# Optimization experiments

Hardware: AMD Instinct MI355X
Metric: run time of the kernel (lower is better)

The kernel has to match this reference:

```python
import jax, jax.numpy as jnp
import numpy as np

NEG = -1e9

def symmetric_quantize(x, bits=8):
    qmax = 2 ** (bits - 1) - 1
    scale = jnp.max(jnp.abs(x)) / qmax
    xq = jnp.clip(jnp.round(x / scale), -(qmax + 1), qmax)
    return xq * scale

def setup_inputs() -> dict:
    key = jax.random.key(0)
    k1, k2, k3, k4, k5 = jax.random.split(key, 5)
    B, S, D = 2, 2048, 1024
    hidden_states = jax.random.normal(k1, (B, S, D), dtype=jnp.float32)
    # additive causal mask [1,1,S,S]
    causal = jnp.tril(jnp.ones((S, S), dtype=bool))
    attention_mask = jnp.where(causal, 0.0, NEG).astype(jnp.float32)[None, None]
    # weights stored (out,in) as used by F.linear; pre-quantized at init (weight_bits=8)
    W_attn = symmetric_quantize(jax.random.normal(k2, (3 * D, D), dtype=jnp.float32) * 0.02)
    b_attn = jax.random.normal(k3, (3 * D,), dtype=jnp.float32) * 0.02
    W_proj = symmetric_quantize(jax.random.normal(k4, (D, D), dtype=jnp.float32) * 0.02)
    b_proj = jax.random.normal(k5, (D,), dtype=jnp.float32) * 0.02
    return {"hidden_states": hidden_states, "attention_mask": attention_mask,
            "W_attn": W_attn, "b_attn": b_attn, "W_proj": W_proj, "b_proj": b_proj}

def reference(hidden_states, attention_mask, W_attn, b_attn, W_proj, b_proj):
    B, S, D = hidden_states.shape
    H = 16
    hd = D // H
    scale = 1.0 / jnp.sqrt(jnp.float32(hd))
    qkv = jnp.einsum('bsd,ed->bse', hidden_states, W_attn) + b_attn  # [B,S,3D]
    q, k, v = jnp.split(qkv, 3, axis=-1)
    def split_heads(x):
        return x.reshape(B, S, H, hd).transpose(0, 2, 1, 3)  # [B,H,S,hd]
    q, k, v = split_heads(q), split_heads(k), split_heads(v)
    # KV-cache fake quant (kv_bits=8)
    k = symmetric_quantize(k)
    v = symmetric_quantize(v)
    present = (k, v)
    scores = jnp.einsum('bhqd,bhkd->bhqk', q, k) * scale + attention_mask
    probs = jax.nn.softmax(scores, axis=-1)  # dropout is identity in eval
    out = jnp.einsum('bhqk,bhkd->bhqd', probs, v)
    out = out.transpose(0, 2, 1, 3).reshape(B, S, D)
    out = symmetric_quantize(out)  # activation fake quant (act_bits=8)
    out = jnp.einsum('bsd,ed->bse', out, W_proj) + b_proj
    return (out, present)
```

## Files before the change

kernel.cpp:

```cpp
#include <hip/hip_runtime.h>
#include <stdint.h>


typedef __attribute__((ext_vector_type(8))) short short8;
typedef __attribute__((ext_vector_type(4))) float floatx4;

#define SSCALE 0.18033688011112042f
#define MASKVAL -30000.0f

__device__ __forceinline__ float bf2f(uint16_t s) {
  return __uint_as_float(((uint32_t)s) << 16);
}
__device__ __forceinline__ uint16_t f2bf(float f) {
  uint32_t u = __float_as_uint(f);
  u += 0x7fffu + ((u >> 16) & 1u);
  return (uint16_t)(u >> 16);
}
__device__ __forceinline__ uint64_t pack4(float a, float b, float c, float d) {
  return (uint64_t)f2bf(a) | ((uint64_t)f2bf(b) << 16) | ((uint64_t)f2bf(c) << 32) |
         ((uint64_t)f2bf(d) << 48);
}
__device__ __forceinline__ float quantize(float v, float inv, float scale) {
  return fminf(fmaxf(rintf(v * inv), -128.f), 127.f) * scale;
}
__device__ __forceinline__ void async_cp16(const void* g, void* l) {
  __builtin_amdgcn_global_load_lds((const __attribute__((address_space(1))) void*)g,
                                   (__attribute__((address_space(3))) void*)l, 16, 0, 0);
}

__global__ void cvt_kernel(const float* __restrict__ hs, const float* __restrict__ wa,
                           const float* __restrict__ wp, uint16_t* __restrict__ hs_b,
                           uint16_t* __restrict__ wa_b, uint16_t* __restrict__ wp_b) {
  const size_t qi = (size_t)blockIdx.x * 256 + threadIdx.x;
  const float* src;
  uint16_t* dst;
  size_t off;
  if (qi < 1048576) {
    src = hs; dst = hs_b; off = qi;
  } else if (qi < 1835008) {
    src = wa; dst = wa_b; off = qi - 1048576;
  } else {
    src = wp; dst = wp_b; off = qi - 1835008;
  }
  const float4 f = ((const float4*)src)[off];
  ((uint64_t*)dst)[off] = pack4(f.x, f.y, f.z, f.w);
}

__global__ __launch_bounds__(256) void gemm_qkv(const uint16_t* __restrict__ A,
                                                const uint16_t* __restrict__ W,
                                                const float* __restrict__ bias,
                                                uint16_t* __restrict__ q_ws,
                                                float* __restrict__ kd,
                                                float* __restrict__ vd,
                                                float* __restrict__ scal) {
  __shared__ uint16_t a_sh[128 * 32];
  __shared__ uint16_t b_sh[128 * 32];
  __shared__ float wred[4];
  const int tid = threadIdx.x;
  const int lane = tid & 63, wid = tid >> 6;
  const int quad = lane >> 4, l16 = lane & 15;
  const int m0 = blockIdx.y * 128, n0 = blockIdx.x * 128;
  const int wrow = (wid >> 1) * 64, wcol = (wid & 1) * 64;
  const uint16_t* Ab = A + (size_t)m0 * 1024;
  const uint16_t* Wb = W + (size_t)n0 * 1024;

  floatx4 acc[4][4] = {};

  for (int k0 = 0; k0 < 1024; k0 += 32) {
#pragma unroll
    for (int i = 0; i < 2; ++i) {
      const int chunk = tid + 256 * i;
      async_cp16(Ab + (size_t)(chunk >> 2) * 1024 + k0 + (chunk & 3) * 8,
                 (char*)a_sh + (size_t)(wid * 64 + 256 * i) * 16);
      async_cp16(Wb + (size_t)(chunk >> 2) * 1024 + k0 + (chunk & 3) * 8,
                 (char*)b_sh + (size_t)(wid * 64 + 256 * i) * 16);
    }
    __syncthreads();
    short8 af[4], bfr[4];
#pragma unroll
    for (int mi = 0; mi < 4; ++mi)
      af[mi] = *(const short8*)&a_sh[(wrow + mi * 16 + l16) * 32 + quad * 8];
#pragma unroll
    for (int ni = 0; ni < 4; ++ni)
      bfr[ni] = *(const short8*)&b_sh[(wcol + ni * 16 + l16) * 32 + quad * 8];
#pragma unroll
    for (int mi = 0; mi < 4; ++mi)
#pragma unroll
      for (int ni = 0; ni < 4; ++ni)
        acc[mi][ni] =
            __builtin_amdgcn_mfma_f32_16x16x32_bf16(af[mi], bfr[ni], acc[mi][ni], 0, 0, 0);
    __syncthreads();
  }

  const int cat = n0 >> 10;
  float tmax = 0.f;
#pragma unroll
  for (int mi = 0; mi < 4; ++mi) {
#pragma unroll
    for (int ni = 0; ni < 4; ++ni) {
      const int col = n0 + wcol + ni * 16 + l16;
      const float bv = bias[col];
#pragma unroll
      for (int r = 0; r < 4; ++r) {
        const int row = m0 + wrow + mi * 16 + quad * 4 + r;
        const float v = acc[mi][ni][r] + bv;
        if (cat == 0) {
          q_ws[(size_t)row * 1024 + col] = f2bf(v * SSCALE);
        } else {
          const int cc = col & 1023, h = cc >> 6, dd = cc & 63;
          const int b = row >> 11, s = row & 2047;
          float* dst = (cat == 1) ? kd : vd;
          dst[(((size_t)b * 16 + h) * 2048 + s) * 64 + dd] = v;
          tmax = fmaxf(tmax, fabsf(v));
        }
      }
    }
  }
  if (cat > 0) {
#pragma unroll
    for (int off = 32; off; off >>= 1) tmax = fmaxf(tmax, __shfl_xor(tmax, off));
    if (lane == 0) wred[wid] = tmax;
    __syncthreads();
    if (tid == 0) {
      const float m = fmaxf(fmaxf(wred[0], wred[1]), fmaxf(wred[2], wred[3]));
      atomicMax((unsigned int*)(scal + (cat - 1)), __float_as_uint(m));
    }
  }
}

__global__ void quant_kv(float* __restrict__ kd, float* __restrict__ vd,
                         const float* __restrict__ scal, uint16_t* __restrict__ kc,
                         uint16_t* __restrict__ vt) {
  __shared__ uint16_t tile[64 * 65];
  const int t = blockIdx.z, bh = blockIdx.y, s0 = blockIdx.x * 64;
  const float mx = t ? scal[1] : scal[0];
  const float scale = mx / 127.f;
  const float inv = (mx > 0.f) ? 127.f / mx : 0.f;
  float* base = (t ? vd : kd) + ((size_t)bh * 2048 + s0) * 64;
  const int tid = threadIdx.x;
#pragma unroll
  for (int i = 0; i < 16; ++i) {
    const int e = tid + 256 * i;
    const float q = quantize(base[e], inv, scale);
    base[e] = q;
    if (t)
      tile[(e >> 6) * 65 + (e & 63)] = f2bf(q);
    else
      kc[((size_t)bh * 2048 + s0) * 64 + e] = f2bf(q);
  }
  if (t) {
    __syncthreads();
#pragma unroll
    for (int i = 0; i < 16; ++i) {
      const int e = tid + 256 * i;
      const int dd = e >> 6, sr = e & 63;
      vt[((size_t)bh * 64 + dd) * 2048 + s0 + sr] = tile[sr * 65 + dd];
    }
  }
}

__global__ __launch_bounds__(512) void attn_kernel(const uint16_t* __restrict__ q_ws,
                                                   const uint16_t* __restrict__ kc,
                                                   const uint16_t* __restrict__ vt,
                                                   uint16_t* __restrict__ at,
                                                   float* __restrict__ omax) {
  __shared__ uint16_t qp_sh[128 * 72];
  __shared__ uint16_t k_sh[2][64 * 72];
  __shared__ uint16_t v_sh[2][64 * 72];
  __shared__ float wred[8];

  const int tid = threadIdx.x, lane = tid & 63, wid = tid >> 6;
  const int quad = lane >> 4, l16 = lane & 15;
  const int pair = blockIdx.x, bh = blockIdx.y;
  const int b = bh >> 4, h = bh & 15;
  const int wq0 = wid * 16;
  const int sr = tid >> 3, sc8 = (tid & 7) * 8;
  const uint16_t* kbase = kc + (size_t)bh * 131072;
  const uint16_t* vtbase = vt + (size_t)bh * 131072;
  float tmax = 0.f;

  for (int phase = 0; phase < 2; ++phase) {
    const int qt = phase ? (15 - pair) : pair;
    const int q0 = qt * 128;
    const int jmax = 2 * qt + 1;

    uint4 kr = *(const uint4*)&kbase[tid * 8];
    uint4 vr = *(const uint4*)&vtbase[(size_t)sr * 2048 + sc8];

#pragma unroll
    for (int i = 0; i < 2; ++i) {
      const int idx = tid + 512 * i;
      const int r = idx >> 3, c8 = (idx & 7) * 8;
      *(uint4*)&qp_sh[r * 72 + c8] =
          *(const uint4*)&q_ws[(size_t)(b * 2048 + q0 + r) * 1024 + h * 64 + c8];
    }
    *(uint4*)&k_sh[0][sr * 72 + sc8] = kr;
    *(uint4*)&v_sh[0][sr * 72 + sc8] = vr;
    __syncthreads();

    short8 qa[2];
#pragma unroll
    for (int ks = 0; ks < 2; ++ks)
      qa[ks] = *(const short8*)&qp_sh[(wq0 + l16) * 72 + ks * 32 + quad * 8];

    floatx4 o[4] = {};
    float mst[4], lst[4];
#pragma unroll
    for (int r = 0; r < 4; ++r) {
      mst[r] = MASKVAL;
      lst[r] = 0.f;
    }

    for (int j = 0; j <= jmax; ++j) {
      const int cur = j & 1;
      uint4 krn, vrn;
      if (j < jmax) {
        krn = *(const uint4*)&kbase[(size_t)(j + 1) * 4096 + tid * 8];
        vrn = *(const uint4*)&vtbase[(size_t)sr * 2048 + (j + 1) * 64 + sc8];
      }

      floatx4 s[4] = {};
#pragma unroll
      for (int ks = 0; ks < 2; ++ks) {
        short8 bfr[4];
#pragma unroll
        for (int ni = 0; ni < 4; ++ni)
          bfr[ni] = *(const short8*)&k_sh[cur][(ni * 16 + l16) * 72 + ks * 32 + quad * 8];
#pragma unroll
        for (int ni = 0; ni < 4; ++ni)
          s[ni] = __builtin_amdgcn_mfma_f32_16x16x32_bf16(qa[ks], bfr[ni], s[ni], 0, 0, 0);
      }

      const bool need_mask = (j >= 2 * qt);
      const int jb = j * 64;
      float mold[4];
      bool chg = false;
#pragma unroll
      for (int r = 0; r < 4; ++r) {
        const int rowg = q0 + wq0 + quad * 4 + r;
        float rmax = MASKVAL;
#pragma unroll
        for (int ni = 0; ni < 4; ++ni) {
          float tt = s[ni][r];
          if (need_mask && (jb + ni * 16 + l16 > rowg)) tt = MASKVAL;
          s[ni][r] = tt;
          rmax = fmaxf(rmax, tt);
        }
#pragma unroll
        for (int msk = 8; msk; msk >>= 1) rmax = fmaxf(rmax, __shfl_xor(rmax, msk));
        mold[r] = mst[r];
        const float mnew = fmaxf(mold[r], rmax);
        mst[r] = mnew;
        chg = chg || (mnew > mold[r]);
      }
      if (__any(chg)) {
#pragma unroll
        for (int r = 0; r < 4; ++r) {
          const float a = exp2f(mold[r] - mst[r]);
          lst[r] *= a;
#pragma unroll
          for (int ni = 0; ni < 4; ++ni) o[ni][r] *= a;
        }
      }
#pragma unroll
      for (int r = 0; r < 4; ++r) {
        const float mn = mst[r];
        uint16_t* prow = &qp_sh[(wq0 + quad * 4 + r) * 72 + l16];
        float rs = 0.f;
#pragma unroll
        for (int ni = 0; ni < 4; ++ni) {
          const float e = exp2f(s[ni][r] - mn);
          rs += e;
          prow[ni * 16] = f2bf(e);
        }
        lst[r] += rs;
      }

#pragma unroll
      for (int ks = 0; ks < 2; ++ks) {
        const short8 pa = *(const short8*)&qp_sh[(wq0 + l16) * 72 + ks * 32 + quad * 8];
        short8 vb[4];
#pragma unroll
        for (int ni = 0; ni < 4; ++ni)
          vb[ni] = *(const short8*)&v_sh[cur][(ni * 16 + l16) * 72 + ks * 32 + quad * 8];
#pragma unroll
        for (int ni = 0; ni < 4; ++ni)
          o[ni] = __builtin_amdgcn_mfma_f32_16x16x32_bf16(pa, vb[ni], o[ni], 0, 0, 0);
      }

      if (j < jmax) {
        *(uint4*)&k_sh[1 - cur][sr * 72 + sc8] = krn;
        *(uint4*)&v_sh[1 - cur][sr * 72 + sc8] = vrn;
      }
      __syncthreads();
    }

#pragma unroll
    for (int r = 0; r < 4; ++r) {
      float l = lst[r];
#pragma unroll
      for (int msk = 8; msk; msk >>= 1) l += __shfl_xor(l, msk);
      const float invl = 1.f / fmaxf(l, 1e-30f);
      const int rowg = q0 + wq0 + quad * 4 + r;
      const size_t rowoff = (size_t)(b * 2048 + rowg) * 1024 + h * 64;
#pragma unroll
      for (int ni = 0; ni < 4; ++ni) {
        const float v = o[ni][r] * invl;
        at[rowoff + ni * 16 + l16] = f2bf(v);
        tmax = fmaxf(tmax, fabsf(v));
      }
    }
  }

#pragma unroll
  for (int off = 32; off; off >>= 1) tmax = fmaxf(tmax, __shfl_xor(tmax, off));
  if (lane == 0) wred[wid] = tmax;
  __syncthreads();
  if (tid == 0) {
    float m = wred[0];
#pragma unroll
    for (int i = 1; i < 8; ++i) m = fmaxf(m, wred[i]);
    atomicMax((unsigned int*)omax, __float_as_uint(m));
  }
}

__global__ void quant_act(uint16_t* __restrict__ a, const float* __restrict__ omax) {
  const size_t i = ((size_t)blockIdx.x * 256 + threadIdx.x) * 8;
  const float mx = *omax;
  const float scale = mx / 127.f;
  const float inv = (mx > 0.f) ? 127.f / mx : 0.f;
  uint16_t v[8];
  *(uint4*)v = *(const uint4*)&a[i];
#pragma unroll
  for (int k = 0; k < 8; ++k) v[k] = f2bf(quantize(bf2f(v[k]), inv, scale));
  *(uint4*)&a[i] = *(const uint4*)v;
}

__global__ __launch_bounds__(256) void gemm_proj(const uint16_t* __restrict__ A,
                                                 const uint16_t* __restrict__ W,
                                                 const float* __restrict__ bias,
                                                 float* __restrict__ C) {
  __shared__ uint16_t a_sh[128 * 32];
  __shared__ uint16_t b_sh[128 * 32];
  const int tid = threadIdx.x;
  const int lane = tid & 63, wid = tid >> 6;
  const int quad = lane >> 4, l16 = lane & 15;
  const int m0 = blockIdx.y * 128, n0 = blockIdx.x * 128;
  const int wrow = (wid >> 1) * 64, wcol = (wid & 1) * 64;
  const uint16_t* Ab = A + (size_t)m0 * 1024;
  const uint16_t* Wb = W + (size_t)n0 * 1024;

  floatx4 acc[4][4] = {};

  for (int k0 = 0; k0 < 1024; k0 += 32) {
#pragma unroll
    for (int i = 0; i < 2; ++i) {
      const int chunk = tid + 256 * i;
      async_cp16(Ab + (size_t)(chunk >> 2) * 1024 + k0 + (chunk & 3) * 8,
                 (char*)a_sh + (size_t)(wid * 64 + 256 * i) * 16);
      async_cp16(Wb + (size_t)(chunk >> 2) * 1024 + k0 + (chunk & 3) * 8,
                 (char*)b_sh + (size_t)(wid * 64 + 256 * i) * 16);
    }
    __syncthreads();
    short8 af[4], bfr[4];
#pragma unroll
    for (int mi = 0; mi < 4; ++mi)
      af[mi] = *(const short8*)&a_sh[(wrow + mi * 16 + l16) * 32 + quad * 8];
#pragma unroll
    for (int ni = 0; ni < 4; ++ni)
      bfr[ni] = *(const short8*)&b_sh[(wcol + ni * 16 + l16) * 32 + quad * 8];
#pragma unroll
    for (int mi = 0; mi < 4; ++mi)
#pragma unroll
      for (int ni = 0; ni < 4; ++ni)
        acc[mi][ni] =
            __builtin_amdgcn_mfma_f32_16x16x32_bf16(af[mi], bfr[ni], acc[mi][ni], 0, 0, 0);
    __syncthreads();
  }

#pragma unroll
  for (int mi = 0; mi < 4; ++mi) {
#pragma unroll
    for (int ni = 0; ni < 4; ++ni) {
      const int col = n0 + wcol + ni * 16 + l16;
      const float bv = bias[col];
#pragma unroll
      for (int r = 0; r < 4; ++r) {
        const int row = m0 + wrow + mi * 16 + quad * 4 + r;
        C[(size_t)row * 1024 + col] = acc[mi][ni][r] + bv;
      }
    }
  }
}

extern "C" void kernel_launch(void* const* d_in, const int* in_sizes, int n_in,
                              void* d_out, int out_size, void* d_ws, size_t ws_size,
                              hipStream_t stream) {
  const float* hs = (const float*)d_in[0];
  const float* Wa = (const float*)d_in[2];
  const float* ba = (const float*)d_in[3];
  const float* Wp = (const float*)d_in[4];
  const float* bp = (const float*)d_in[5];

  float* outd = (float*)d_out;
  float* kd = outd + (size_t)4194304;
  float* vd = outd + (size_t)8388608;

  char* ws = (char*)d_ws;
  const size_t MB = 1024 * 1024;
  uint16_t* hs_b = (uint16_t*)ws;
  uint16_t* Wa_b = (uint16_t*)(ws + 8 * MB);
  uint16_t* Wp_b = (uint16_t*)(ws + 14 * MB);
  uint16_t* q_ws = (uint16_t*)(ws + 16 * MB);
  uint16_t* kc = (uint16_t*)(ws + 24 * MB);
  uint16_t* vt = (uint16_t*)(ws + 32 * MB);
  uint16_t* at = (uint16_t*)(ws + 40 * MB);
  float* scal = (float*)(ws + 48 * MB);

  hipMemsetAsync(scal, 0, 4 * sizeof(float), stream);
  cvt_kernel<<<8192, 256, 0, stream>>>(hs, Wa, Wp, hs_b, Wa_b, Wp_b);
  gemm_qkv<<<dim3(24, 32), 256, 0, stream>>>(hs_b, Wa_b, ba, q_ws, kd, vd, scal);
  quant_kv<<<dim3(32, 32, 2), 256, 0, stream>>>(kd, vd, scal, kc, vt);
  attn_kernel<<<dim3(8, 32), 512, 0, stream>>>(q_ws, kc, vt, at, scal + 2);
  quant_act<<<2048, 256, 0, stream>>>(at, scal + 2);
  gemm_proj<<<dim3(8, 32), 256, 0, stream>>>(at, Wp_b, bp, outd);
}
```

Before: 245.6 us.

## Split attention into one tile per block with transposed MFMA and lazy rescale

Each block now handles one 128-row query tile instead of a balanced pair of tiles, doubling the grid to 16x32. Tiles are ordered heaviest-first, with the order alternating between batches, to help load balance. The MFMA operands are swapped so each lane owns one query row. This turns row reductions into two cross-quad shuffles and allows packed bf16 stores of P via v_cvt_pk_bf16_f32. Warps whose rows lie entirely before a key block skip its compute, and the online-softmax rescale is deferred until the max grows by more than 8 (in log2 units), trading a looser bound on exp values for fewer rescales.

```diff
diff --git a/kernel.cpp b/kernel.cpp
--- a/kernel.cpp
+++ b/kernel.cpp
@@ -171,145 +171,140 @@
 
   const int tid = threadIdx.x, lane = tid & 63, wid = tid >> 6;
   const int quad = lane >> 4, l16 = lane & 15;
-  const int pair = blockIdx.x, bh = blockIdx.y;
+  const int qt = (blockIdx.y & 16) ? (int)blockIdx.x : (15 - (int)blockIdx.x);
+  const int bh = blockIdx.y;
   const int b = bh >> 4, h = bh & 15;
   const int wq0 = wid * 16;
   const int sr = tid >> 3, sc8 = (tid & 7) * 8;
   const uint16_t* kbase = kc + (size_t)bh * 131072;
   const uint16_t* vtbase = vt + (size_t)bh * 131072;
-  float tmax = 0.f;
-
-  for (int phase = 0; phase < 2; ++phase) {
-    const int qt = phase ? (15 - pair) : pair;
-    const int q0 = qt * 128;
-    const int jmax = 2 * qt + 1;
-
-    uint4 kr = *(const uint4*)&kbase[tid * 8];
-    uint4 vr = *(const uint4*)&vtbase[(size_t)sr * 2048 + sc8];
-
-#pragma unroll
-    for (int i = 0; i < 2; ++i) {
-      const int idx = tid + 512 * i;
-      const int r = idx >> 3, c8 = (idx & 7) * 8;
-      *(uint4*)&qp_sh[r * 72 + c8] =
-          *(const uint4*)&q_ws[(size_t)(b * 2048 + q0 + r) * 1024 + h * 64 + c8];
-    }
-    *(uint4*)&k_sh[0][sr * 72 + sc8] = kr;
-    *(uint4*)&v_sh[0][sr * 72 + sc8] = vr;
-    __syncthreads();
-
-    short8 qa[2];
-#pragma unroll
-    for (int ks = 0; ks < 2; ++ks)
-      qa[ks] = *(const short8*)&qp_sh[(wq0 + l16) * 72 + ks * 32 + quad * 8];
-
-    floatx4 o[4] = {};
-    float mst[4], lst[4];
-#pragma unroll
-    for (int r = 0; r < 4; ++r) {
-      mst[r] = MASKVAL;
-      lst[r] = 0.f;
-    }
-
-    for (int j = 0; j <= jmax; ++j) {
-      const int cur = j & 1;
-      uint4 krn, vrn;
-      if (j < jmax) {
-        krn = *(const uint4*)&kbase[(size_t)(j + 1) * 4096 + tid * 8];
-        vrn = *(const uint4*)&vtbase[(size_t)sr * 2048 + (j + 1) * 64 + sc8];
-      }
-
+
+  const int q0 = qt * 128;
+  const int jmax = 2 * qt + 1;
+  const int rowg = q0 + wq0 + l16;
+
+  uint4 kr = *(const uint4*)&kbase[tid * 8];
+  uint4 vr = *(const uint4*)&vtbase[(size_t)sr * 2048 + sc8];
+
+#pragma unroll
+  for (int i = 0; i < 2; ++i) {
+    const int idx = tid + 512 * i;
+    const int r = idx >> 3, c8 = (idx & 7) * 8;
+    *(uint4*)&qp_sh[r * 72 + c8] =
+        *(const uint4*)&q_ws[(size_t)(b * 2048 + q0 + r) * 1024 + h * 64 + c8];
+  }
+  *(uint4*)&k_sh[0][sr * 72 + sc8] = kr;
+  *(uint4*)&v_sh[0][sr * 72 + sc8] = vr;
+  __syncthreads();
+
+  short8 qa[2];
+#pragma unroll
+  for (int ks = 0; ks < 2; ++ks)
+    qa[ks] = *(const short8*)&qp_sh[(wq0 + l16) * 72 + ks * 32 + quad * 8];
+
+  uint16_t* prow = &qp_sh[(wq0 + l16) * 72];
+
+  floatx4 o[4] = {};
+  float mst = MASKVAL, lst = 0.f;
+
+  for (int j = 0; j <= jmax; ++j) {
+    const int cur = j & 1;
+    uint4 krn, vrn;
+    if (j < jmax) {
+      krn = *(const uint4*)&kbase[(size_t)(j + 1) * 4096 + tid * 8];
+      vrn = *(const uint4*)&vtbase[(size_t)sr * 2048 + (j + 1) * 64 + sc8];
+    }
+
+    const int jb = j * 64;
+    if (jb <= q0 + wq0 + 15) {
       floatx4 s[4] = {};
 #pragma unroll
       for (int ks = 0; ks < 2; ++ks) {
-        short8 bfr[4];
+        short8 kf[4];
 #pragma unroll
         for (int ni = 0; ni < 4; ++ni)
-          bfr[ni] = *(const short8*)&k_sh[cur][(ni * 16 + l16) * 72 + ks * 32 + quad * 8];
+          kf[ni] = *(const short8*)&k_sh[cur][(ni * 16 + l16) * 72 + ks * 32 + quad * 8];
 #pragma unroll
         for (int ni = 0; ni < 4; ++ni)
-          s[ni] = __builtin_amdgcn_mfma_f32_16x16x32_bf16(qa[ks], bfr[ni], s[ni], 0, 0, 0);
+          s[ni] = __builtin_amdgcn_mfma_f32_16x16x32_bf16(kf[ni], qa[ks], s[ni], 0, 0, 0);
       }
 
       const bool need_mask = (j >= 2 * qt);
-      const int jb = j * 64;
-      float mold[4];
-      bool chg = false;
-#pragma unroll
-      for (int r = 0; r < 4; ++r) {
-        const int rowg = q0 + wq0 + quad * 4 + r;
-        float rmax = MASKVAL;
-#pragma unroll
-        for (int ni = 0; ni < 4; ++ni) {
+      float rmax = MASKVAL;
+#pragma unroll
+      for (int ni = 0; ni < 4; ++ni) {
+#pragma unroll
+        for (int r = 0; r < 4; ++r) {
           float tt = s[ni][r];
-          if (need_mask && (jb + ni * 16 + l16 > rowg)) tt = MASKVAL;
+          if (need_mask && (jb + ni * 16 + quad * 4 + r > rowg)) tt = MASKVAL;
           s[ni][r] = tt;
           rmax = fmaxf(rmax, tt);
         }
-#pragma unroll
-        for (int msk = 8; msk; msk >>= 1) rmax = fmaxf(rmax, __shfl_xor(rmax, msk));
-        mold[r] = mst[r];
-        const float mnew = fmaxf(mold[r], rmax);
-        mst[r] = mnew;
-        chg = chg || (mnew > mold[r]);
-      }
-      if (__any(chg)) {
-#pragma unroll
-        for (int r = 0; r < 4; ++r) {
-          const float a = exp2f(mold[r] - mst[r]);
-          lst[r] *= a;
-#pragma unroll
-          for (int ni = 0; ni < 4; ++ni) o[ni][r] *= a;
-        }
-      }
-#pragma unroll
-      for (int r = 0; r < 4; ++r) {
-        const float mn = mst[r];
-        uint16_t* prow = &qp_sh[(wq0 + quad * 4 + r) * 72 + l16];
-        float rs = 0.f;
-#pragma unroll
-        for (int ni = 0; ni < 4; ++ni) {
-          const float e = exp2f(s[ni][r] - mn);
-          rs += e;
-          prow[ni * 16] = f2bf(e);
-        }
-        lst[r] += rs;
+      }
+      rmax = fmaxf(rmax, __shfl_xor(rmax, 16));
+      rmax = fmaxf(rmax, __shfl_xor(rmax, 32));
+
+      if (__any(rmax > mst + 8.f)) {
+        const float mnew = fmaxf(mst, rmax);
+        const float a = exp2f(mst - mnew);
+        lst *= a;
+#pragma unroll
+        for (int ni = 0; ni < 4; ++ni)
+#pragma unroll
+          for (int r = 0; r < 4; ++r) o[ni][r] *= a;
+        mst = mnew;
+      }
+
+#pragma unroll
+      for (int ni = 0; ni < 4; ++ni) {
+        const float e0 = exp2f(s[ni][0] - mst);
+        const float e1 = exp2f(s[ni][1] - mst);
+        const float e2 = exp2f(s[ni][2] - mst);
+        const float e3 = exp2f(s[ni][3] - mst);
+        lst += (e0 + e1) + (e2 + e3);
+        uint32_t w0, w1;
+        asm("v_cvt_pk_bf16_f32 %0, %1, %2" : "=v"(w0) : "v"(e0), "v"(e1));
+        asm("v_cvt_pk_bf16_f32 %0, %1, %2" : "=v"(w1) : "v"(e2), "v"(e3));
+        uint2 pw;
+        pw.x = w0;
+        pw.y = w1;
+        *(uint2*)((char*)prow + ni * 32 + quad * 8) = pw;
       }
 
 #pragma unroll
       for (int ks = 0; ks < 2; ++ks) {
-        const short8 pa = *(const short8*)&qp_sh[(wq0 + l16) * 72 + ks * 32 + quad * 8];
-        short8 vb[4];
+        const short8 pb = *(const short8*)((char*)prow + ks * 64 + quad * 16);
+        short8 vf[4];
 #pragma unroll
         for (int ni = 0; ni < 4; ++ni)
-          vb[ni] = *(const short8*)&v_sh[cur][(ni * 16 + l16) * 72 + ks * 32 + quad * 8];
+          vf[ni] = *(const short8*)&v_sh[cur][(ni * 16 + l16) * 72 + ks * 32 + quad * 8];
 #pragma unroll
         for (int ni = 0; ni < 4; ++ni)
-          o[ni] = __builtin_amdgcn_mfma_f32_16x16x32_bf16(pa, vb[ni], o[ni], 0, 0, 0);
-      }
-
-      if (j < jmax) {
-        *(uint4*)&k_sh[1 - cur][sr * 72 + sc8] = krn;
-        *(uint4*)&v_sh[1 - cur][sr * 72 + sc8] = vrn;
-      }
-      __syncthreads();
-    }
-
-#pragma unroll
-    for (int r = 0; r < 4; ++r) {
-      float l = lst[r];
-#pragma unroll
-      for (int msk = 8; msk; msk >>= 1) l += __shfl_xor(l, msk);
-      const float invl = 1.f / fmaxf(l, 1e-30f);
-      const int rowg = q0 + wq0 + quad * 4 + r;
-      const size_t rowoff = (size_t)(b * 2048 + rowg) * 1024 + h * 64;
-#pragma unroll
-      for (int ni = 0; ni < 4; ++ni) {
-        const float v = o[ni][r] * invl;
-        at[rowoff + ni * 16 + l16] = f2bf(v);
-        tmax = fmaxf(tmax, fabsf(v));
-      }
-    }
+          o[ni] = __builtin_amdgcn_mfma_f32_16x16x32_bf16(vf[ni], pb, o[ni], 0, 0, 0);
+      }
+    }
+
+    if (j < jmax) {
+      *(uint4*)&k_sh[1 - cur][sr * 72 + sc8] = krn;
+      *(uint4*)&v_sh[1 - cur][sr * 72 + sc8] = vrn;
+    }
+    __syncthreads();
+  }
+
+  float l = lst;
+  l += __shfl_xor(l, 16);
+  l += __shfl_xor(l, 32);
+  const float invl = 1.f / fmaxf(l, 1e-30f);
+  const size_t rowoff = (size_t)(b * 2048 + rowg) * 1024 + h * 64;
+  float tmax = 0.f;
+#pragma unroll
+  for (int ni = 0; ni < 4; ++ni) {
+    const float v0 = o[ni][0] * invl;
+    const float v1 = o[ni][1] * invl;
+    const float v2 = o[ni][2] * invl;
+    const float v3 = o[ni][3] * invl;
+    tmax = fmaxf(tmax, fmaxf(fmaxf(fabsf(v0), fabsf(v1)), fmaxf(fabsf(v2), fabsf(v3))));
+    *(uint64_t*)&at[rowoff + ni * 16 + quad * 4] = pack4(v0, v1, v2, v3);
   }
 
 #pragma unroll
@@ -421,7 +416,7 @@
   cvt_kernel<<<8192, 256, 0, stream>>>(hs, Wa, Wp, hs_b, Wa_b, Wp_b);
   gemm_qkv<<<dim3(24, 32), 256, 0, stream>>>(hs_b, Wa_b, ba, q_ws, kd, vd, scal);
   quant_kv<<<dim3(32, 32, 2), 256, 0, stream>>>(kd, vd, scal, kc, vt);
-  attn_kernel<<<dim3(8, 32), 512, 0, stream>>>(q_ws, kc, vt, at, scal + 2);
+  attn_kernel<<<dim3(16, 32), 512, 0, stream>>>(q_ws, kc, vt, at, scal + 2);
   quant_act<<<2048, 256, 0, stream>>>(at, scal + 2);
   gemm_proj<<<dim3(8, 32), 256, 0, stream>>>(at, Wp_b, bp, outd);
 }
```

After: 229.7 us. 1.07x faster.
